# Kernel tuning notes

Hardware: AMD Instinct MI355X
Metric: run time of the kernel (lower is better)

The kernel has to match this reference:

```python
import jax, jax.numpy as jnp
import numpy as np

B, NQ, NK = 4, 2048, 2048
QDIM = CDIM = 1024
H, DH = 16, 64  # heads, dim_head; inner_dim = H*DH = 1024
SCALE = DH ** -0.5
WSTD = 0.02


def setup_inputs() -> dict:
    key = jax.random.key(0)
    ks = jax.random.split(key, 6)
    inner = H * DH
    return {
        "x": jax.random.normal(ks[0], (B, NQ, QDIM), dtype=jnp.float32),
        "context": jax.random.normal(ks[1], (B, NK, CDIM), dtype=jnp.float32),
        "Wq": jax.random.normal(ks[2], (inner, QDIM), dtype=jnp.float32) * WSTD,
        "Wk": jax.random.normal(ks[3], (inner, CDIM), dtype=jnp.float32) * WSTD,
        "Wv": jax.random.normal(ks[4], (inner, CDIM), dtype=jnp.float32) * WSTD,
        "Wo": jax.random.normal(ks[5], (QDIM, inner), dtype=jnp.float32) * WSTD,
        "bo": jnp.zeros((QDIM,), dtype=jnp.float32),
    }


def reference(x, context, Wq, Wk, Wv, Wo, bo):
    b, nq, _ = x.shape
    nk = context.shape[1]
    # Linear projections (torch Linear: y = x @ W.T)
    q = (x @ Wq.T).reshape(b, nq, H, DH)        # b n h d
    k = (context @ Wk.T).reshape(b, nk, H, DH)
    v = (context @ Wv.T).reshape(b, nk, H, DH)
    # sim = Q K^T * scale, materialized as in the original einsum
    sim = jnp.einsum('bihd,bjhd->bhij', q, k) * SCALE
    attn = jax.nn.softmax(sim, axis=-1)
    out = jnp.einsum('bhij,bjhd->bihd', attn, v).reshape(b, nq, H * DH)
    return out @ Wo.T + bo
```

## Files before the change

kernel.cpp:

```cpp
#include <hip/hip_runtime.h>
#include <cstdint>
#include <cstddef>


typedef __attribute__((ext_vector_type(8))) short short8;
typedef __attribute__((ext_vector_type(4))) float f32x4;
typedef __attribute__((ext_vector_type(4))) unsigned short ushort4v;

#define GLD16(gsrc, ldst) \
  __builtin_amdgcn_global_load_lds((const __attribute__((address_space(1))) unsigned int*)(gsrc), \
                                   (__attribute__((address_space(3))) unsigned int*)(ldst), 16, 0, 0)

__device__ __forceinline__ unsigned short f32_to_bf16(float f) {
  unsigned int u = __builtin_bit_cast(unsigned int, f);
  u += 0x7FFFu + ((u >> 16) & 1u);
  return (unsigned short)(u >> 16);
}

__device__ __forceinline__ unsigned int cvtpk_bf16(float lo, float hi) {
  unsigned int r;
  asm("v_cvt_pk_bf16_f32 %0, %1, %2" : "=v"(r) : "v"(lo), "v"(hi));
  return r;
}

__device__ __forceinline__ float exp2_fast(float x) {
#if __has_builtin(__builtin_amdgcn_exp2f)
  return __builtin_amdgcn_exp2f(x);
#else
  return exp2f(x);
#endif
}

__global__ __launch_bounds__(256) void cvt_x2(const float* __restrict__ x,
                                              const float* __restrict__ ctx,
                                              unsigned short* __restrict__ xb,
                                              unsigned short* __restrict__ cb) {
  const int seg = blockIdx.x >> 11;
  const float* in = seg ? ctx : x;
  unsigned short* out = seg ? cb : xb;
  int i = (blockIdx.x & 2047) * 256 + threadIdx.x;
  const int stride = 2048 * 256;
#pragma unroll
  for (int k = 0; k < 4; ++k, i += stride) {
    float4 v = reinterpret_cast<const float4*>(in)[i];
    ushort4v o;
    o.x = f32_to_bf16(v.x);
    o.y = f32_to_bf16(v.y);
    o.z = f32_to_bf16(v.z);
    o.w = f32_to_bf16(v.w);
    reinterpret_cast<ushort4v*>(out)[i] = o;
  }
}

__global__ __launch_bounds__(256) void cvt_w4(const float* __restrict__ a, const float* __restrict__ b,
                                              const float* __restrict__ c, const float* __restrict__ d,
                                              unsigned short* __restrict__ oa, unsigned short* __restrict__ ob,
                                              unsigned short* __restrict__ oc, unsigned short* __restrict__ od,
                                              float scale_a) {
  int seg = blockIdx.x >> 8;
  int blk = blockIdx.x & 255;
  const float* in = seg == 0 ? a : seg == 1 ? b : seg == 2 ? c : d;
  unsigned short* out = seg == 0 ? oa : seg == 1 ? ob : seg == 2 ? oc : od;
  float sc = seg == 0 ? scale_a : 1.0f;
  int i = blk * 256 + threadIdx.x;
#pragma unroll
  for (int k = 0; k < 4; ++k, i += 65536) {
    float4 v = reinterpret_cast<const float4*>(in)[i];
    ushort4v o;
    o.x = f32_to_bf16(v.x * sc);
    o.y = f32_to_bf16(v.y * sc);
    o.z = f32_to_bf16(v.z * sc);
    o.w = f32_to_bf16(v.w * sc);
    reinterpret_cast<ushort4v*>(out)[i] = o;
  }
}

template<bool BF16_OUT, bool BIAS>
__device__ __forceinline__ void gemm_core(const unsigned short* __restrict__ A,
                                          const unsigned short* __restrict__ Bm,
                                          void* __restrict__ Cout,
                                          const float* __restrict__ bias,
                                          int M, int N, int K, int bx, int by,
                                          unsigned short* smA, unsigned short* smB) {
  const int t    = threadIdx.x;
  const int lane = t & 63;
  const int wid  = t >> 6;
  const int l15  = lane & 15;
  const int l16  = lane >> 4;
  const int m0   = by * 128;
  const int n0   = bx * 128;
  const int wr   = (wid >> 1) * 64;
  const int wc   = (wid & 1) * 64;

  f32x4 acc[4][4];
#pragma unroll
  for (int i = 0; i < 4; ++i)
#pragma unroll
    for (int j = 0; j < 4; ++j) acc[i][j] = (f32x4){0.f, 0.f, 0.f, 0.f};

  const char* Abase = (const char*)A + (size_t)m0 * K * 2;
  const char* Bbase = (const char*)Bm + (size_t)n0 * K * 2;

  auto stageG = [&](int bufi, int k0) {
#pragma unroll
    for (int i = 0; i < 2; ++i) {
      int g = i * 256 + t;
      int r = g >> 2, c = g & 3;
      int cs = c ^ ((r >> 1) & 3);
      GLD16(Abase + (size_t)r * (K * 2) + (size_t)k0 * 2 + cs * 16,
            (char*)smA + bufi * 8192 + (g & ~63) * 16);
      GLD16(Bbase + (size_t)r * (K * 2) + (size_t)k0 * 2 + cs * 16,
            (char*)smB + bufi * 8192 + (g & ~63) * 16);
    }
  };

  const int nk = K >> 5;
  stageG(0, 0);
  asm volatile("s_waitcnt vmcnt(0)" ::: "memory");
  __builtin_amdgcn_s_barrier();

  for (int t0 = 0; t0 < nk; ++t0) {
    const int bufi = t0 & 1;
    if (t0 + 1 < nk) stageG(bufi ^ 1, (t0 + 1) * 32);

    short8 af[4], bfv[4];
#pragma unroll
    for (int mi = 0; mi < 4; ++mi) {
      int row = wr + mi * 16 + l15;
      int cs = l16 ^ ((row >> 1) & 3);
      af[mi] = *reinterpret_cast<const short8*>((const char*)smA + bufi * 8192 + row * 64 + cs * 16);
    }
#pragma unroll
    for (int ni = 0; ni < 4; ++ni) {
      int row = wc + ni * 16 + l15;
      int cs = l16 ^ ((row >> 1) & 3);
      bfv[ni] = *reinterpret_cast<const short8*>((const char*)smB + bufi * 8192 + row * 64 + cs * 16);
    }
    __builtin_amdgcn_s_setprio(1);
#pragma unroll
    for (int mi = 0; mi < 4; ++mi)
#pragma unroll
      for (int ni = 0; ni < 4; ++ni)
        acc[mi][ni] = __builtin_amdgcn_mfma_f32_16x16x32_bf16(af[mi], bfv[ni], acc[mi][ni], 0, 0, 0);
    __builtin_amdgcn_s_setprio(0);

    asm volatile("s_waitcnt vmcnt(0)" ::: "memory");
    __builtin_amdgcn_s_barrier();
  }

#pragma unroll
  for (int mi = 0; mi < 4; ++mi)
#pragma unroll
    for (int ni = 0; ni < 4; ++ni)
#pragma unroll
      for (int r = 0; r < 4; ++r) {
        int row = m0 + wr + mi * 16 + l16 * 4 + r;
        int col = n0 + wc + ni * 16 + l15;
        float v = acc[mi][ni][r];
        if (BIAS) v += bias[col];
        if (BF16_OUT)
          ((unsigned short*)Cout)[(size_t)row * N + col] = f32_to_bf16(v);
        else
          ((float*)Cout)[(size_t)row * N + col] = v;
      }
}

template<bool BF16_OUT, bool BIAS>
__global__ __launch_bounds__(256) void gemm_bt(const unsigned short* __restrict__ A,
                                               const unsigned short* __restrict__ Bm,
                                               void* __restrict__ Cout,
                                               const float* __restrict__ bias,
                                               int M, int N, int K) {
  __shared__ __align__(16) unsigned short smA[2 * 128 * 32];
  __shared__ __align__(16) unsigned short smB[2 * 128 * 32];
  gemm_core<BF16_OUT, BIAS>(A, Bm, Cout, bias, M, N, K, blockIdx.x, blockIdx.y, smA, smB);
}

__global__ __launch_bounds__(256) void gemm3(const unsigned short* __restrict__ xb,
                                             const unsigned short* __restrict__ cb,
                                             const unsigned short* __restrict__ wqb,
                                             const unsigned short* __restrict__ wkb,
                                             const unsigned short* __restrict__ wvb,
                                             unsigned short* __restrict__ Qb,
                                             unsigned short* __restrict__ Kb,
                                             unsigned short* __restrict__ Vtb) {
  __shared__ __align__(16) unsigned short smA[2 * 128 * 32];
  __shared__ __align__(16) unsigned short smB[2 * 128 * 32];
  const int id = blockIdx.x;
  if (id < 512) {
    gemm_core<true, false>(xb, wqb, Qb, nullptr, 8192, 1024, 1024, id & 7, id >> 3, smA, smB);
  } else if (id < 1024) {
    int l = id - 512;
    gemm_core<true, false>(cb, wkb, Kb, nullptr, 8192, 1024, 1024, l & 7, l >> 3, smA, smB);
  } else {
    int l = id - 1024;
    gemm_core<true, false>(wvb, cb, Vtb, nullptr, 1024, 8192, 1024, l & 63, l >> 6, smA, smB);
  }
}

__global__ __launch_bounds__(256, 3) void flash_attn(const unsigned short* __restrict__ Q,
                                                     const unsigned short* __restrict__ Kb,
                                                     const unsigned short* __restrict__ Vt,
                                                     unsigned short* __restrict__ O) {
  __shared__ __align__(16) unsigned short smK[2][64 * 64];
  __shared__ __align__(16) unsigned short smV[2][64 * 64];
  __shared__ __align__(16) unsigned int   smP[4][32 * 36];

  const int t    = threadIdx.x;
  const int lane = t & 63;
  const int wid  = t >> 6;
  const int l15  = lane & 15;
  const int l16  = lane >> 4;
  const int qt   = blockIdx.x;
  const int h    = blockIdx.y;
  const int b    = blockIdx.z;

  const char* Kbase = (const char*)Kb + ((size_t)(b * 2048) * 1024 + h * 64) * 2;
  const char* Vbase = (const char*)Vt + ((size_t)(h * 64) * 8192 + b * 2048) * 2;
  unsigned int* smPw = &smP[wid][0];

  auto stage = [&](int buf, int j0) {
#pragma unroll
    for (int i = 0; i < 2; ++i) {
      int g = i * 256 + t;
      int r = g >> 3, c = g & 7;
      int cs = c ^ (r & 7);
      const char* srcK = Kbase + (size_t)(j0 + r) * 2048 + cs * 16;
      const char* srcV = Vbase + (size_t)r * 16384 + (size_t)j0 * 2 + cs * 16;
      GLD16(srcK, (char*)&smK[buf][0] + (g & ~63) * 16);
      GLD16(srcV, (char*)&smV[buf][0] + (g & ~63) * 16);
    }
  };

  stage(0, 0);

  short8 qf[2][2];
#pragma unroll
  for (int qg = 0; qg < 2; ++qg)
#pragma unroll
    for (int kk = 0; kk < 2; ++kk) {
      size_t idx = (size_t)(b * 2048 + qt * 128 + wid * 32 + qg * 16 + l15) * 1024
                 + (size_t)h * 64 + kk * 32 + l16 * 8;
      qf[qg][kk] = *reinterpret_cast<const short8*>(&Q[idx]);
    }

  f32x4 accO[2][4];
  float m_run[2], l_run[2];
#pragma unroll
  for (int qg = 0; qg < 2; ++qg) {
    m_run[qg] = -1.0e30f;
    l_run[qg] = 0.f;
#pragma unroll
    for (int di = 0; di < 4; ++di) accO[qg][di] = (f32x4){0.f, 0.f, 0.f, 0.f};
  }

  asm volatile("s_waitcnt vmcnt(0)" ::: "memory");
  __builtin_amdgcn_s_barrier();

  for (int jt = 0; jt < 32; ++jt) {
    const int buf = jt & 1;
    if (jt < 31) stage(buf ^ 1, (jt + 1) * 64);

    short8 kf[4][2];
#pragma unroll
    for (int kc = 0; kc < 4; ++kc)
#pragma unroll
      for (int kk = 0; kk < 2; ++kk) {
        int row = kc * 16 + l15;
        int cs = (kk * 4 + l16) ^ (row & 7);
        kf[kc][kk] = *reinterpret_cast<const short8*>((const char*)&smK[buf][0] + row * 128 + cs * 16);
      }
    f32x4 s[2][4];
    const f32x4 z = (f32x4){0.f, 0.f, 0.f, 0.f};
    __builtin_amdgcn_s_setprio(1);
#pragma unroll
    for (int qg = 0; qg < 2; ++qg)
#pragma unroll
      for (int kc = 0; kc < 4; ++kc) {
        f32x4 tmp = __builtin_amdgcn_mfma_f32_16x16x32_bf16(kf[kc][0], qf[qg][0], z, 0, 0, 0);
        s[qg][kc] = __builtin_amdgcn_mfma_f32_16x16x32_bf16(kf[kc][1], qf[qg][1], tmp, 0, 0, 0);
      }
    __builtin_amdgcn_s_setprio(0);

    short8 vf[4][2];
#pragma unroll
    for (int di = 0; di < 4; ++di)
#pragma unroll
      for (int kk = 0; kk < 2; ++kk) {
        int row = di * 16 + l15;
        int cs = (kk * 4 + l16) ^ (row & 7);
        vf[di][kk] = *reinterpret_cast<const short8*>((const char*)&smV[buf][0] + row * 128 + cs * 16);
      }

#pragma unroll
    for (int qg = 0; qg < 2; ++qg) {
      float vmax = s[qg][0][0];
#pragma unroll
      for (int kc = 0; kc < 4; ++kc)
#pragma unroll
        for (int r = 0; r < 4; ++r) vmax = fmaxf(vmax, s[qg][kc][r]);
      vmax = fmaxf(vmax, __shfl_xor(vmax, 16));
      vmax = fmaxf(vmax, __shfl_xor(vmax, 32));

      if (__any(vmax > m_run[qg] + 11.5f)) {
        float mnew = fmaxf(m_run[qg], vmax);
        float alpha = exp2_fast(m_run[qg] - mnew);
        m_run[qg] = mnew;
        l_run[qg] *= alpha;
        int av = __builtin_bit_cast(int, alpha);
#pragma unroll
        for (int r = 0; r < 4; ++r) {
          float at = __builtin_bit_cast(float, __builtin_amdgcn_ds_bpermute((l16 * 4 + r) * 4, av));
#pragma unroll
          for (int di = 0; di < 4; ++di) accO[qg][di][r] *= at;
        }
      }

      float rsum = 0.f;
#pragma unroll
      for (int kc = 0; kc < 4; ++kc)
#pragma unroll
        for (int r = 0; r < 4; ++r) {
          float p = exp2_fast(s[qg][kc][r] - m_run[qg]);
          s[qg][kc][r] = p;
          rsum += p;
        }
      rsum += __shfl_xor(rsum, 16);
      rsum += __shfl_xor(rsum, 32);
      l_run[qg] += rsum;

#pragma unroll
      for (int kc = 0; kc < 4; ++kc) {
        unsigned int w0 = cvtpk_bf16(s[qg][kc][0], s[qg][kc][1]);
        unsigned int w1 = cvtpk_bf16(s[qg][kc][2], s[qg][kc][3]);
        int word = (qg * 16 + l15) * 36 + kc * 8 + l16 * 2;
        *reinterpret_cast<uint2*>(&smPw[word]) = uint2{w0, w1};
      }
    }

    asm volatile("s_waitcnt lgkmcnt(0)" ::: "memory");
    __builtin_amdgcn_sched_barrier(0);

    short8 pf[2][2];
#pragma unroll
    for (int qg = 0; qg < 2; ++qg)
#pragma unroll
      for (int kk = 0; kk < 2; ++kk) {
        int word = (qg * 16 + l15) * 36 + kk * 16 + l16 * 4;
        pf[qg][kk] = *reinterpret_cast<const short8*>(&smPw[word]);
      }

    __builtin_amdgcn_s_setprio(1);
#pragma unroll
    for (int qg = 0; qg < 2; ++qg)
#pragma unroll
      for (int di = 0; di < 4; ++di) {
        accO[qg][di] = __builtin_amdgcn_mfma_f32_16x16x32_bf16(pf[qg][0], vf[di][0], accO[qg][di], 0, 0, 0);
        accO[qg][di] = __builtin_amdgcn_mfma_f32_16x16x32_bf16(pf[qg][1], vf[di][1], accO[qg][di], 0, 0, 0);
      }
    __builtin_amdgcn_s_setprio(0);

    asm volatile("s_waitcnt vmcnt(0)" ::: "memory");
    __builtin_amdgcn_s_barrier();
  }

#pragma unroll
  for (int qg = 0; qg < 2; ++qg) {
    float inv = 1.f / l_run[qg];
    int iv = __builtin_bit_cast(int, inv);
#pragma unroll
    for (int r = 0; r < 4; ++r) {
      float it = __builtin_bit_cast(float, __builtin_amdgcn_ds_bpermute((l16 * 4 + r) * 4, iv));
      int row = b * 2048 + qt * 128 + wid * 32 + qg * 16 + l16 * 4 + r;
#pragma unroll
      for (int di = 0; di < 4; ++di) {
        int col = h * 64 + di * 16 + l15;
        O[(size_t)row * 1024 + col] = f32_to_bf16(accO[qg][di][r] * it);
      }
    }
  }
}

extern "C" void kernel_launch(void* const* d_in, const int* in_sizes, int n_in,
                              void* d_out, int out_size, void* d_ws, size_t ws_size,
                              hipStream_t stream) {
  (void)in_sizes; (void)n_in; (void)out_size; (void)ws_size;
  const float* x   = (const float*)d_in[0];
  const float* ctx = (const float*)d_in[1];
  const float* Wq  = (const float*)d_in[2];
  const float* Wk  = (const float*)d_in[3];
  const float* Wv  = (const float*)d_in[4];
  const float* Wo  = (const float*)d_in[5];
  const float* bo  = (const float*)d_in[6];
  float* out = (float*)d_out;

  char* ws = (char*)d_ws;
  const size_t MB = 1024 * 1024;
  unsigned short* xb  = (unsigned short*)(ws + 0);
  unsigned short* cb  = (unsigned short*)(ws + 16 * MB);
  unsigned short* Qb  = (unsigned short*)(ws + 32 * MB);
  unsigned short* Kb  = (unsigned short*)(ws + 48 * MB);
  unsigned short* Vtb = (unsigned short*)(ws + 64 * MB);
  unsigned short* wqb = (unsigned short*)(ws + 80 * MB);
  unsigned short* wkb = (unsigned short*)(ws + 82 * MB);
  unsigned short* wvb = (unsigned short*)(ws + 84 * MB);
  unsigned short* wob = (unsigned short*)(ws + 86 * MB);
  unsigned short* Ob  = xb;

  const float SCALE_LOG2E = 0.125f * 1.4426950408889634f;

  cvt_x2<<<4096, 256, 0, stream>>>(x, ctx, xb, cb);
  cvt_w4<<<1024, 256, 0, stream>>>(Wq, Wk, Wv, Wo, wqb, wkb, wvb, wob, SCALE_LOG2E);

  gemm3<<<1536, 256, 0, stream>>>(xb, cb, wqb, wkb, wvb, Qb, Kb, Vtb);

  flash_attn<<<dim3(2048/128, 16, 4), 256, 0, stream>>>(Qb, Kb, Vtb, Ob);

  gemm_bt<false, true><<<dim3(1024/128, 8192/128), 256, 0, stream>>>(Ob, wob, out, bo, 8192, 1024, 1024);
}
```

Baseline: 339.5 us.

## Triple-buffer GEMM LDS pipeline and remap block IDs for XCD locality

The GEMM core moves from double to triple buffering in LDS. It prefetches two k-tiles ahead and waits with a partial vmcnt, so each iteration needs a single barrier instead of a full drain plus barrier. Block indices in the projection and output GEMMs are also remapped so that consecutive blocks sharing the same operands land on the same XCD (orig&7 chiplet interleave), aiming at better L2 reuse. The cost is 50% more LDS per block, which could reduce occupancy.

```diff
diff --git a/kernel.cpp b/kernel.cpp
--- a/kernel.cpp
+++ b/kernel.cpp
@@ -116,12 +116,17 @@
 
   const int nk = K >> 5;
   stageG(0, 0);
-  asm volatile("s_waitcnt vmcnt(0)" ::: "memory");
-  __builtin_amdgcn_s_barrier();
+  stageG(1, 32);
 
   for (int t0 = 0; t0 < nk; ++t0) {
-    const int bufi = t0 & 1;
-    if (t0 + 1 < nk) stageG(bufi ^ 1, (t0 + 1) * 32);
+    const int bufi = t0 % 3;
+    if (t0 < nk - 1) { asm volatile("s_waitcnt vmcnt(4)" ::: "memory"); }
+    else             { asm volatile("s_waitcnt vmcnt(0)" ::: "memory"); }
+    __builtin_amdgcn_s_barrier();
+    if (t0 + 2 < nk) {
+      int bn = bufi + 2; if (bn >= 3) bn -= 3;
+      stageG(bn, (t0 + 2) * 32);
+    }
 
     short8 af[4], bfv[4];
 #pragma unroll
@@ -143,9 +148,6 @@
       for (int ni = 0; ni < 4; ++ni)
         acc[mi][ni] = __builtin_amdgcn_mfma_f32_16x16x32_bf16(af[mi], bfv[ni], acc[mi][ni], 0, 0, 0);
     __builtin_amdgcn_s_setprio(0);
-
-    asm volatile("s_waitcnt vmcnt(0)" ::: "memory");
-    __builtin_amdgcn_s_barrier();
   }
 
 #pragma unroll
@@ -165,15 +167,15 @@
       }
 }
 
-template<bool BF16_OUT, bool BIAS>
-__global__ __launch_bounds__(256) void gemm_bt(const unsigned short* __restrict__ A,
-                                               const unsigned short* __restrict__ Bm,
-                                               void* __restrict__ Cout,
-                                               const float* __restrict__ bias,
-                                               int M, int N, int K) {
-  __shared__ __align__(16) unsigned short smA[2 * 128 * 32];
-  __shared__ __align__(16) unsigned short smB[2 * 128 * 32];
-  gemm_core<BF16_OUT, BIAS>(A, Bm, Cout, bias, M, N, K, blockIdx.x, blockIdx.y, smA, smB);
+__global__ __launch_bounds__(256) void gemm_o(const unsigned short* __restrict__ Ob,
+                                              const unsigned short* __restrict__ wob,
+                                              float* __restrict__ out,
+                                              const float* __restrict__ bo) {
+  __shared__ __align__(16) unsigned short smA[3 * 128 * 32];
+  __shared__ __align__(16) unsigned short smB[3 * 128 * 32];
+  const int orig = blockIdx.x;
+  const int wgid = (orig & 7) * 64 + (orig >> 3);
+  gemm_core<false, true>(Ob, wob, out, bo, 8192, 1024, 1024, wgid & 7, wgid >> 3, smA, smB);
 }
 
 __global__ __launch_bounds__(256) void gemm3(const unsigned short* __restrict__ xb,
@@ -184,9 +186,10 @@
                                              unsigned short* __restrict__ Qb,
                                              unsigned short* __restrict__ Kb,
                                              unsigned short* __restrict__ Vtb) {
-  __shared__ __align__(16) unsigned short smA[2 * 128 * 32];
-  __shared__ __align__(16) unsigned short smB[2 * 128 * 32];
-  const int id = blockIdx.x;
+  __shared__ __align__(16) unsigned short smA[3 * 128 * 32];
+  __shared__ __align__(16) unsigned short smB[3 * 128 * 32];
+  const int orig = blockIdx.x;
+  const int id = (orig & 7) * 192 + (orig >> 3);
   if (id < 512) {
     gemm_core<true, false>(xb, wqb, Qb, nullptr, 8192, 1024, 1024, id & 7, id >> 3, smA, smB);
   } else if (id < 1024) {
@@ -416,5 +419,5 @@
 
   flash_attn<<<dim3(2048/128, 16, 4), 256, 0, stream>>>(Qb, Kb, Vtb, Ob);
 
-  gemm_bt<false, true><<<dim3(1024/128, 8192/128), 256, 0, stream>>>(Ob, wob, out, bo, 8192, 1024, 1024);
-}
+  gemm_o<<<512, 256, 0, stream>>>(Ob, wob, out, bo);
+}
```

Result: no change. 339.3 us (-0.1%).
